# Performance work log

Measured on AMD Instinct MI355X. Metric: run time of the kernel, lower is better.

Reference implementation:

```python
import jax, jax.numpy as jnp
import numpy as np

NEG_SLOPE = 0.2
BN_EPS = 1e-5


def _gatv2(x, src, dst, Wl, Wr, att, b, N, concat):
    # x: [N, Cin]; src/dst: [E] (self-loops already appended)
    H, F = att.shape
    xl = (x @ Wl).reshape(N, H, F)  # source transform
    xr = (x @ Wr).reshape(N, H, F)  # target transform
    s = jax.nn.leaky_relu(xl[src] + xr[dst], NEG_SLOPE)  # [E,H,F]
    e = jnp.einsum('ehf,hf->eh', s, att)                  # [E,H]
    m = jax.ops.segment_max(e, dst, num_segments=N)       # [N,H]
    ex = jnp.exp(e - m[dst])
    den = jax.ops.segment_sum(ex, dst, num_segments=N)
    alpha = ex / den[dst]                                 # [E,H] softmax over in-edges
    out = jax.ops.segment_sum(alpha[:, :, None] * xl[src], dst, num_segments=N)  # [N,H,F]
    out = out.reshape(N, H * F) if concat else out.mean(axis=1)
    return out + b


def _bn_eval(x, g, b, rm, rv):
    return (x - rm) * jax.lax.rsqrt(rv + BN_EPS) * g + b


def setup_inputs() -> dict:
    key = jax.random.key(0)
    ks = jax.random.split(key, 16)
    N, E, Cin, Fh, H, Cout = 50000, 800000, 128, 64, 4, 128
    Hm = H * Fh  # 256
    d = {
        'x': jax.random.normal(ks[0], (N, Cin), jnp.float32),
        'edge_index': jax.random.randint(ks[1], (2, E), 0, N, jnp.int64),
        'Wl1': jax.random.normal(ks[2], (Cin, Hm), jnp.float32) / np.sqrt(Cin),
        'Wr1': jax.random.normal(ks[3], (Cin, Hm), jnp.float32) / np.sqrt(Cin),
        'att1': jax.random.normal(ks[4], (H, Fh), jnp.float32) / np.sqrt(Fh),
        'b1': jnp.zeros((Hm,), jnp.float32),
        'bn1_g': jax.random.uniform(ks[5], (Hm,), jnp.float32, 0.5, 1.5),
        'bn1_b': 0.1 * jax.random.normal(ks[6], (Hm,), jnp.float32),
        'bn1_m': jnp.zeros((Hm,), jnp.float32),
        'bn1_v': jnp.ones((Hm,), jnp.float32),
        'Wl2': jax.random.normal(ks[7], (Hm, Hm), jnp.float32) / np.sqrt(Hm),
        'Wr2': jax.random.normal(ks[8], (Hm, Hm), jnp.float32) / np.sqrt(Hm),
        'att2': jax.random.normal(ks[9], (H, Fh), jnp.float32) / np.sqrt(Fh),
        'b2': jnp.zeros((Hm,), jnp.float32),
        'bn2_g': jax.random.uniform(ks[10], (Hm,), jnp.float32, 0.5, 1.5),
        'bn2_b': 0.1 * jax.random.normal(ks[11], (Hm,), jnp.float32),
        'bn2_m': jnp.zeros((Hm,), jnp.float32),
        'bn2_v': jnp.ones((Hm,), jnp.float32),
        'Wl3': jax.random.normal(ks[12], (Hm, Cout), jnp.float32) / np.sqrt(Hm),
        'Wr3': jax.random.normal(ks[13], (Hm, Cout), jnp.float32) / np.sqrt(Hm),
        'att3': jax.random.normal(ks[14], (1, Cout), jnp.float32) / np.sqrt(Cout),
        'b3': jnp.zeros((Cout,), jnp.float32),
    }
    return d


def reference(x, edge_index, Wl1, Wr1, att1, b1, bn1_g, bn1_b, bn1_m, bn1_v,
              Wl2, Wr2, att2, b2, bn2_g, bn2_b, bn2_m, bn2_v,
              Wl3, Wr3, att3, b3):
    N = x.shape[0]
    loop = jnp.arange(N, dtype=edge_index.dtype)
    src = jnp.concatenate([edge_index[0], loop])  # add self-loops (PyG default)
    dst = jnp.concatenate([edge_index[1], loop])
    h = _gatv2(x, src, dst, Wl1, Wr1, att1, b1, N, True)
    h = jax.nn.elu(_bn_eval(h, bn1_g, bn1_b, bn1_m, bn1_v))  # dropout=identity (eval)
    h = _gatv2(h, src, dst, Wl2, Wr2, att2, b2, N, True)
    h = jax.nn.elu(_bn_eval(h, bn2_g, bn2_b, bn2_m, bn2_v))
    return _gatv2(h, src, dst, Wl3, Wr3, att3, b3, N, False)
```

## Files before the change

### kernel.cpp

```cpp
#include <hip/hip_runtime.h>
#include <math.h>

#define NEG_SLOPE 0.2f
#define BN_EPS 1e-5f
#define LOG2E 1.44269504f

typedef _Float16 f16x8 __attribute__((ext_vector_type(8)));
typedef float f32x4 __attribute__((ext_vector_type(4)));
typedef _Float16 h2 __attribute__((ext_vector_type(2)));

union F8 { f16x8 v; h2 h[4]; _Float16 s[8]; uint4 u; };

__device__ __forceinline__ void async_copy16(const void* g, void* l) {
  __builtin_amdgcn_global_load_lds(
      (const __attribute__((address_space(1))) void*)g,
      (__attribute__((address_space(3))) void*)l, 16, 0, 0);
}

__device__ __forceinline__ unsigned int pack2f(float a, float b) {
  union { unsigned int u; _Float16 h[2]; } c;
  c.h[0] = (_Float16)a; c.h[1] = (_Float16)b; return c.u;
}

__device__ __forceinline__ float fdot2f(h2 a, h2 b, float c) {
#if __has_builtin(__builtin_amdgcn_fdot2)
  return __builtin_amdgcn_fdot2(a, b, c, false);
#else
  return fmaf((float)a[0], (float)b[0], fmaf((float)a[1], (float)b[1], c));
#endif
}

template <int CTRL>
__device__ __forceinline__ float dpp_xadd(float x) {
  int yi = __builtin_amdgcn_mov_dpp(__builtin_bit_cast(int, x), CTRL, 0xF, 0xF, true);
  return x + __builtin_bit_cast(float, yi);
}

__global__ void k_zero_i32(int* __restrict__ p, int n) {
  int i = blockIdx.x * blockDim.x + threadIdx.x;
  if (i < n) p[i] = 0;
}

__global__ void k_f2h(const float* __restrict__ in, unsigned int* __restrict__ out, int n2) {
  int i = blockIdx.x * blockDim.x + threadIdx.x;
  if (i < n2) {
    float2 v = reinterpret_cast<const float2*>(in)[i];
    out[i] = pack2f(v.x, v.y);
  }
}

__global__ __launch_bounds__(256) void k_prep_w3(
    const float* __restrict__ Wl1, const float* __restrict__ Wr1,
    const float* __restrict__ Wl2, const float* __restrict__ Wr2,
    const float* __restrict__ Wl3, const float* __restrict__ Wr3,
    int Cin, int Hm, int Cout,
    _Float16* __restrict__ WT1, _Float16* __restrict__ WT2, _Float16* __restrict__ WT3) {
  int i = blockIdx.x * 256 + threadIdx.x;
  int n1 = 2 * Hm * Cin, n2 = 2 * Hm * Hm, n3 = 2 * Cout * Hm;
  if (i < n1) {
    int c = i / Cin, k = i % Cin;
    float v = (c < Hm) ? Wl1[(size_t)k * Hm + c] : Wr1[(size_t)k * Hm + (c - Hm)];
    WT1[i] = (_Float16)v;
    return;
  }
  i -= n1;
  if (i < n2) {
    int c = i / Hm, k = i % Hm;
    float v = (c < Hm) ? Wl2[(size_t)k * Hm + c] : Wr2[(size_t)k * Hm + (c - Hm)];
    WT2[i] = (_Float16)v;
    return;
  }
  i -= n2;
  if (i < n3) {
    int c = i / Hm, k = i % Hm;
    float v = (c < Cout) ? Wl3[(size_t)k * Cout + c] : Wr3[(size_t)k * Cout + (c - Cout)];
    WT3[i] = (_Float16)v;
  }
}

__global__ __launch_bounds__(256) void k_prep_misc(
    const float* __restrict__ att1, const float* __restrict__ att2, const float* __restrict__ att3,
    const float* __restrict__ b1, const float* __restrict__ g1, const float* __restrict__ bb1,
    const float* __restrict__ m1, const float* __restrict__ v1,
    const float* __restrict__ b2, const float* __restrict__ g2, const float* __restrict__ bb2,
    const float* __restrict__ m2, const float* __restrict__ v2,
    _Float16* __restrict__ a16_1, _Float16* __restrict__ a16_2, _Float16* __restrict__ a16_3,
    float* __restrict__ sc1, float* __restrict__ sh1,
    float* __restrict__ sc2, float* __restrict__ sh2) {
  int c = threadIdx.x;
  a16_1[c] = (_Float16)(att1[c] * LOG2E);
  a16_2[c] = (_Float16)(att2[c] * LOG2E);
  if (c < 128) a16_3[c] = (_Float16)(att3[c] * LOG2E);
  float s = g1[c] * rsqrtf(v1[c] + BN_EPS);
  sc1[c] = s; sh1[c] = (b1[c] - m1[c]) * s + bb1[c];
  s = g2[c] * rsqrtf(v2[c] + BN_EPS);
  sc2[c] = s; sh2[c] = (b2[c] - m2[c]) * s + bb2[c];
}

__global__ void k_count(const int* __restrict__ ei, int E, int N, int* __restrict__ deg) {
  int e = blockIdx.x * blockDim.x + threadIdx.x;
  int T = E + N;
  if (e >= T) return;
  int d = (e < E) ? ei[E + e] : (e - E);
  atomicAdd(&deg[d], 1);
}

__global__ __launch_bounds__(256) void k_bsum(const int* __restrict__ deg, int N,
                                              int* __restrict__ bsum) {
  int t = threadIdx.x;
  int i = blockIdx.x * 256 + t;
  int v = (i < N) ? deg[i] : 0;
  #pragma unroll
  for (int off = 32; off > 0; off >>= 1) v += __shfl_xor(v, off, 64);
  __shared__ int ws[4];
  if ((t & 63) == 0) ws[t >> 6] = v;
  __syncthreads();
  if (t == 0) bsum[blockIdx.x] = ws[0] + ws[1] + ws[2] + ws[3];
}

__global__ __launch_bounds__(1024) void k_bscan(int* __restrict__ bsum, int nb, int N,
                                                int* __restrict__ offs) {
  int t = threadIdx.x;
  int lane = t & 63, w = t >> 6;
  int v = (t < nb) ? bsum[t] : 0;
  int val = v;
  #pragma unroll
  for (int off = 1; off < 64; off <<= 1) {
    int x = __shfl_up(val, off, 64);
    if (lane >= off) val += x;
  }
  __shared__ int ws[16];
  if (lane == 63) ws[w] = val;
  __syncthreads();
  if (w == 0) {
    int s = (lane < 16) ? ws[lane] : 0;
    #pragma unroll
    for (int off = 1; off < 16; off <<= 1) {
      int x = __shfl_up(s, off, 64);
      if (lane >= off) s += x;
    }
    if (lane < 16) ws[lane] = s;
  }
  __syncthreads();
  int excl = (w > 0 ? ws[w - 1] : 0) + val - v;
  if (t < nb) bsum[t] = excl;
  if (t == nb - 1) offs[N] = excl + v;
}

__global__ __launch_bounds__(256) void k_boffs(const int* __restrict__ deg, int N,
                                               const int* __restrict__ bpre,
                                               int* __restrict__ offs, int* __restrict__ cursor) {
  int t = threadIdx.x;
  int i = blockIdx.x * 256 + t;
  int lane = t & 63, w = t >> 6;
  int v = (i < N) ? deg[i] : 0;
  int val = v;
  #pragma unroll
  for (int off = 1; off < 64; off <<= 1) {
    int x = __shfl_up(val, off, 64);
    if (lane >= off) val += x;
  }
  __shared__ int ws[4];
  if (lane == 63) ws[w] = val;
  __syncthreads();
  int wo = 0;
  #pragma unroll
  for (int k = 0; k < 4; ++k) if (k < w) wo += ws[k];
  int excl = bpre[blockIdx.x] + wo + val - v;
  if (i < N) { offs[i] = excl; cursor[i] = excl; }
}

__global__ void k_scatter(const int* __restrict__ ei, int E, int N,
                          int* __restrict__ cursor, int* __restrict__ csr_src) {
  int e = blockIdx.x * blockDim.x + threadIdx.x;
  int T = E + N;
  if (e < 32) csr_src[T + e] = 0;
  if (e >= T) return;
  int s, d;
  if (e < E) { s = ei[e]; d = ei[E + e]; } else { s = d = e - E; }
  int pos = atomicAdd(&cursor[d], 1);
  csr_src[pos] = s;
}

__global__ __launch_bounds__(512) void k_hgemm(const _Float16* __restrict__ A,
                                               const _Float16* __restrict__ BT,
                                               _Float16* __restrict__ C,
                                               int M, int Ntot, int K) {
  __shared__ _Float16 As[2][128 * 64];
  __shared__ _Float16 Bs[2][256 * 64];
  const int t = threadIdx.x;
  const int lane = t & 63, w = t >> 6;
  const int wr = w >> 2, wc = w & 3;
  const int bm0 = blockIdx.x * 128, bn0 = blockIdx.y * 256;
  f32x4 acc[4][4] = {};
  const int nkt = K >> 6;

  auto stage = [&](int b, int kt) {
    #pragma unroll
    for (int i = 0; i < 2; ++i) {
      int q = i * 512 + t;
      int row = q >> 3, sl = q & 7;
      int ssrc = sl ^ (row & 7);
      int ga = bm0 + row; if (ga >= M) ga = M - 1;
      async_copy16(&A[(size_t)ga * K + kt * 64 + ssrc * 8], &As[b][q * 8]);
    }
    #pragma unroll
    for (int i = 0; i < 4; ++i) {
      int q = i * 512 + t;
      int row = q >> 3, sl = q & 7;
      int ssrc = sl ^ (row & 7);
      async_copy16(&BT[(size_t)(bn0 + row) * K + kt * 64 + ssrc * 8], &Bs[b][q * 8]);
    }
  };

  stage(0, 0);
  for (int kt = 0; kt < nkt; ++kt) {
    int cur = kt & 1;
    if (kt + 1 < nkt) {
      stage(cur ^ 1, kt + 1);
      asm volatile("s_waitcnt vmcnt(6)" ::: "memory");
    } else {
      asm volatile("s_waitcnt vmcnt(0)" ::: "memory");
    }
    __builtin_amdgcn_s_barrier();
    #pragma unroll
    for (int ks = 0; ks < 2; ++ks) {
      f16x8 a[4], b[4];
      const int sl = ks * 4 + (lane >> 4);
      #pragma unroll
      for (int mi = 0; mi < 4; ++mi) {
        int row = wr * 64 + mi * 16 + (lane & 15);
        a[mi] = *(const f16x8*)&As[cur][(row * 8 + (sl ^ (row & 7))) * 8];
      }
      #pragma unroll
      for (int ni = 0; ni < 4; ++ni) {
        int row = wc * 64 + ni * 16 + (lane & 15);
        b[ni] = *(const f16x8*)&Bs[cur][(row * 8 + (sl ^ (row & 7))) * 8];
      }
      #pragma unroll
      for (int mi = 0; mi < 4; ++mi)
        #pragma unroll
        for (int ni = 0; ni < 4; ++ni)
          acc[mi][ni] = __builtin_amdgcn_mfma_f32_16x16x32_f16(a[mi], b[ni], acc[mi][ni], 0, 0, 0);
    }
    __builtin_amdgcn_s_barrier();
  }
  const int r0 = (lane >> 4) * 4;
  const int cc = lane & 15;
  #pragma unroll
  for (int mi = 0; mi < 4; ++mi) {
    #pragma unroll
    for (int r = 0; r < 4; ++r) {
      int row = bm0 + wr * 64 + mi * 16 + r0 + r;
      if (row >= M) continue;
      #pragma unroll
      for (int ni = 0; ni < 4; ++ni) {
        int col = bn0 + wc * 64 + ni * 16 + cc;
        C[(size_t)row * Ntot + col] = (_Float16)acc[mi][ni][r];
      }
    }
  }
}

__global__ __launch_bounds__(256) void k_gat4(
    const _Float16* __restrict__ xlr,
    const _Float16* __restrict__ att16,
    const float* __restrict__ sc, const float* __restrict__ sh,
    const int* __restrict__ offs, const int* __restrict__ csr,
    int N, _Float16* __restrict__ hout) {
  const int n = blockIdx.x * 4 + (threadIdx.x >> 6);
  if (n >= N) return;
  const int lane = threadIdx.x & 63;
  const int sub = lane & 15;
  const int qi = lane >> 4;
  const unsigned subB = (unsigned)sub << 5;
  const char* __restrict__ xc = (const char*)xlr;

  F8 at0, at1, xr0, xr1;
  at0.u = *(const uint4*)((const char*)att16 + subB);
  at1.u = *(const uint4*)((const char*)att16 + subB + 16);
  {
    unsigned xro = (unsigned)n * 1024u + 512u + subB;
    xr0.u = *(const uint4*)(xc + xro);
    xr1.u = *(const uint4*)(xc + xro + 16);
  }
  const h2 k02 = {(_Float16)NEG_SLOPE, (_Float16)NEG_SLOPE};
  const int j0 = offs[n], j1 = offs[n + 1];

  float m = -INFINITY, l = 0.f;
  float acc[16];
  #pragma unroll
  for (int i = 0; i < 16; ++i) acc[i] = 0.f;

  unsigned oA = (unsigned)csr[j0 + qi] * 1024u + subB;
  unsigned oB = (unsigned)csr[j0 + 4 + qi] * 1024u + subB;
  F8 v0, v1;
  v0.u = *(const uint4*)(xc + oA);
  v1.u = *(const uint4*)(xc + oA + 16);

  for (int j = j0; j < j1; j += 4) {
    F8 n0, n1;
    n0.u = *(const uint4*)(xc + oB);
    n1.u = *(const uint4*)(xc + oB + 16);
    oB = (unsigned)csr[j + 8 + qi] * 1024u + subB;

    float e = 0.f;
    #pragma unroll
    for (int r = 0; r < 4; ++r) {
      h2 s0 = v0.h[r] + xr0.h[r];
      s0 = __builtin_elementwise_max(s0, s0 * k02);
      e = fdot2f(s0, at0.h[r], e);
      h2 s1 = v1.h[r] + xr1.h[r];
      s1 = __builtin_elementwise_max(s1, s1 * k02);
      e = fdot2f(s1, at1.h[r], e);
    }
    e = dpp_xadd<0xB1>(e);
    e = dpp_xadd<0x4E>(e);
    if (j + qi >= j1) e = -1e30f;

    if (__any(e > m + 11.5f)) {
      float mc = fmaxf(m, e);
      mc = fmaxf(mc, __shfl_xor(mc, 16, 64));
      mc = fmaxf(mc, __shfl_xor(mc, 32, 64));
      float c0 = exp2f(m - mc);
      l *= c0;
      #pragma unroll
      for (int i = 0; i < 16; ++i) acc[i] *= c0;
      m = mc;
    }
    float p = exp2f(e - m);
    l += p;
    #pragma unroll
    for (int i = 0; i < 8; ++i) acc[i] = fmaf(p, (float)v0.s[i], acc[i]);
    #pragma unroll
    for (int i = 0; i < 8; ++i) acc[8 + i] = fmaf(p, (float)v1.s[i], acc[8 + i]);
    v0 = n0; v1 = n1;
  }
  l += __shfl_xor(l, 16, 64);
  l += __shfl_xor(l, 32, 64);
  #pragma unroll
  for (int i = 0; i < 16; ++i) {
    acc[i] += __shfl_xor(acc[i], 16, 64);
    acc[i] += __shfl_xor(acc[i], 32, 64);
  }
  if (qi == 0) {
    float inv = 1.f / l;
    const float4* sc4 = (const float4*)sc;
    const float4* sh4 = (const float4*)sh;
    float ov[16];
    #pragma unroll
    for (int k = 0; k < 4; ++k) {
      float4 s4 = sc4[4 * sub + k], t4 = sh4[4 * sub + k];
      ov[4 * k + 0] = acc[4 * k + 0] * inv * s4.x + t4.x;
      ov[4 * k + 1] = acc[4 * k + 1] * inv * s4.y + t4.y;
      ov[4 * k + 2] = acc[4 * k + 2] * inv * s4.z + t4.z;
      ov[4 * k + 3] = acc[4 * k + 3] * inv * s4.w + t4.w;
    }
    #pragma unroll
    for (int i = 0; i < 16; ++i) ov[i] = ov[i] > 0.f ? ov[i] : (__expf(ov[i]) - 1.f);
    F8 o0, o1;
    #pragma unroll
    for (int i = 0; i < 8; ++i) { o0.s[i] = (_Float16)ov[i]; o1.s[i] = (_Float16)ov[8 + i]; }
    F8* ob = (F8*)hout;
    ob[(size_t)n * 32 + 2 * sub] = o0;
    ob[(size_t)n * 32 + 2 * sub + 1] = o1;
  }
}

__global__ __launch_bounds__(256) void k_gat1(
    const _Float16* __restrict__ xlr,
    const _Float16* __restrict__ att16,
    const float* __restrict__ bias,
    const int* __restrict__ offs, const int* __restrict__ csr,
    int N, float* __restrict__ out) {
  const int n = blockIdx.x * 4 + (threadIdx.x >> 6);
  if (n >= N) return;
  const int lane = threadIdx.x & 63;
  const int sub = lane & 7;
  const int gi = lane >> 3;
  const unsigned subB = (unsigned)sub << 5;
  const char* __restrict__ xc = (const char*)xlr;

  F8 at0, at1, xr0, xr1;
  at0.u = *(const uint4*)((const char*)att16 + subB);
  at1.u = *(const uint4*)((const char*)att16 + subB + 16);
  {
    unsigned xro = (unsigned)n * 512u + 256u + subB;
    xr0.u = *(const uint4*)(xc + xro);
    xr1.u = *(const uint4*)(xc + xro + 16);
  }
  const h2 k02 = {(_Float16)NEG_SLOPE, (_Float16)NEG_SLOPE};
  const int j0 = offs[n], j1 = offs[n + 1];

  float m = -INFINITY, l = 0.f;
  float acc[16];
  #pragma unroll
  for (int i = 0; i < 16; ++i) acc[i] = 0.f;

  unsigned oA = (unsigned)csr[j0 + gi] * 512u + subB;
  unsigned oB = (unsigned)csr[j0 + 8 + gi] * 512u + subB;
  F8 v0, v1;
  v0.u = *(const uint4*)(xc + oA);
  v1.u = *(const uint4*)(xc + oA + 16);

  for (int j = j0; j < j1; j += 8) {
    F8 n0, n1;
    n0.u = *(const uint4*)(xc + oB);
    n1.u = *(const uint4*)(xc + oB + 16);
    oB = (unsigned)csr[j + 16 + gi] * 512u + subB;

    float e = 0.f;
    #pragma unroll
    for (int r = 0; r < 4; ++r) {
      h2 s0 = v0.h[r] + xr0.h[r];
      s0 = __builtin_elementwise_max(s0, s0 * k02);
      e = fdot2f(s0, at0.h[r], e);
      h2 s1 = v1.h[r] + xr1.h[r];
      s1 = __builtin_elementwise_max(s1, s1 * k02);
      e = fdot2f(s1, at1.h[r], e);
    }
    e = dpp_xadd<0xB1>(e);
    e = dpp_xadd<0x4E>(e);
    e += __shfl_xor(e, 4, 64);
    if (j + gi >= j1) e = -1e30f;

    if (__any(e > m + 11.5f)) {
      float mc = fmaxf(m, e);
      mc = fmaxf(mc, __shfl_xor(mc, 8, 64));
      mc = fmaxf(mc, __shfl_xor(mc, 16, 64));
      mc = fmaxf(mc, __shfl_xor(mc, 32, 64));
      float c0 = exp2f(m - mc);
      l *= c0;
      #pragma unroll
      for (int i = 0; i < 16; ++i) acc[i] *= c0;
      m = mc;
    }
    float p = exp2f(e - m);
    l += p;
    #pragma unroll
    for (int i = 0; i < 8; ++i) acc[i] = fmaf(p, (float)v0.s[i], acc[i]);
    #pragma unroll
    for (int i = 0; i < 8; ++i) acc[8 + i] = fmaf(p, (float)v1.s[i], acc[8 + i]);
    v0 = n0; v1 = n1;
  }
  l += __shfl_xor(l, 8, 64);
  l += __shfl_xor(l, 16, 64);
  l += __shfl_xor(l, 32, 64);
  #pragma unroll
  for (int i = 0; i < 16; ++i) {
    acc[i] += __shfl_xor(acc[i], 8, 64);
    acc[i] += __shfl_xor(acc[i], 16, 64);
    acc[i] += __shfl_xor(acc[i], 32, 64);
  }
  if (gi == 0) {
    float inv = 1.f / l;
    const float4* b4 = (const float4*)bias;
    float4* ob = (float4*)out;
    #pragma unroll
    for (int k = 0; k < 4; ++k) {
      float4 bb = b4[4 * sub + k];
      float4 o;
      o.x = acc[4 * k + 0] * inv + bb.x;
      o.y = acc[4 * k + 1] * inv + bb.y;
      o.z = acc[4 * k + 2] * inv + bb.z;
      o.w = acc[4 * k + 3] * inv + bb.w;
      ob[(size_t)n * 32 + 4 * sub + k] = o;
    }
  }
}

extern "C" void kernel_launch(void* const* d_in, const int* in_sizes, int n_in,
                              void* d_out, int out_size, void* d_ws, size_t ws_size,
                              hipStream_t stream) {
  const float* x    = (const float*)d_in[0];
  const int*   ei   = (const int*)d_in[1];
  const float* Wl1  = (const float*)d_in[2];
  const float* Wr1  = (const float*)d_in[3];
  const float* att1 = (const float*)d_in[4];
  const float* b1   = (const float*)d_in[5];
  const float* bn1g = (const float*)d_in[6];
  const float* bn1b = (const float*)d_in[7];
  const float* bn1m = (const float*)d_in[8];
  const float* bn1v = (const float*)d_in[9];
  const float* Wl2  = (const float*)d_in[10];
  const float* Wr2  = (const float*)d_in[11];
  const float* att2 = (const float*)d_in[12];
  const float* b2   = (const float*)d_in[13];
  const float* bn2g = (const float*)d_in[14];
  const float* bn2b = (const float*)d_in[15];
  const float* bn2m = (const float*)d_in[16];
  const float* bn2v = (const float*)d_in[17];
  const float* Wl3  = (const float*)d_in[18];
  const float* Wr3  = (const float*)d_in[19];
  const float* att3 = (const float*)d_in[20];
  const float* b3   = (const float*)d_in[21];

  const int Hm   = in_sizes[5];
  const int Cout = in_sizes[21];
  const int Cin  = in_sizes[2] / Hm;
  const int N    = in_sizes[0] / Cin;
  const int E    = in_sizes[1] / 2;
  const int T    = E + N;

  _Float16* x16 = (_Float16*)d_ws;
  _Float16* h   = x16 + (size_t)N * Cin;
  _Float16* xlr = h + (size_t)N * Hm;
  _Float16* WT1 = xlr + (size_t)N * 2 * Hm;
  _Float16* WT2 = WT1 + (size_t)2 * Hm * Cin;
  _Float16* WT3 = WT2 + (size_t)2 * Hm * Hm;
  _Float16* a16_1 = WT3 + (size_t)2 * Cout * Hm;
  _Float16* a16_2 = a16_1 + 256;
  _Float16* a16_3 = a16_2 + 256;
  float* sc1 = (float*)(a16_3 + 128);
  float* sh1 = sc1 + 256;
  float* sc2 = sh1 + 256;
  float* sh2 = sc2 + 256;
  int* deg    = (int*)(sh2 + 256);
  int* offs   = deg + N;
  int* cursor = offs + N + 1;
  int* csr    = cursor + N;
  int* bsum   = csr + T + 32;

  const int nb = (N + 255) / 256;

  k_zero_i32<<<(N + 255) / 256, 256, 0, stream>>>(deg, N);
  k_count<<<(T + 255) / 256, 256, 0, stream>>>(ei, E, N, deg);
  k_bsum<<<nb, 256, 0, stream>>>(deg, N, bsum);
  k_bscan<<<1, 1024, 0, stream>>>(bsum, nb, N, offs);
  k_boffs<<<nb, 256, 0, stream>>>(deg, N, bsum, offs, cursor);
  k_scatter<<<(T + 255) / 256, 256, 0, stream>>>(ei, E, N, cursor, csr);

  int n2 = N * Cin / 2;
  k_f2h<<<(n2 + 255) / 256, 256, 0, stream>>>(x, (unsigned int*)x16, n2);
  int wtot = 2 * Hm * Cin + 2 * Hm * Hm + 2 * Cout * Hm;
  k_prep_w3<<<(wtot + 255) / 256, 256, 0, stream>>>(Wl1, Wr1, Wl2, Wr2, Wl3, Wr3,
                                                    Cin, Hm, Cout, WT1, WT2, WT3);
  k_prep_misc<<<1, 256, 0, stream>>>(att1, att2, att3,
                                     b1, bn1g, bn1b, bn1m, bn1v,
                                     b2, bn2g, bn2b, bn2m, bn2v,
                                     a16_1, a16_2, a16_3, sc1, sh1, sc2, sh2);

  const int mb = (N + 127) / 128;
  const int gb = (N + 3) / 4;

  k_hgemm<<<dim3(mb, 2 * Hm / 256), 512, 0, stream>>>(x16, WT1, xlr, N, 2 * Hm, Cin);
  k_gat4<<<gb, 256, 0, stream>>>(xlr, a16_1, sc1, sh1, offs, csr, N, h);

  k_hgemm<<<dim3(mb, 2 * Hm / 256), 512, 0, stream>>>(h, WT2, xlr, N, 2 * Hm, Hm);
  k_gat4<<<gb, 256, 0, stream>>>(xlr, a16_2, sc2, sh2, offs, csr, N, h);

  k_hgemm<<<dim3(mb, 2 * Cout / 256), 512, 0, stream>>>(h, WT3, xlr, N, 2 * Cout, Hm);
  k_gat1<<<gb, 256, 0, stream>>>(xlr, a16_3, b3, offs, csr, N, (float*)d_out);
}
```

Measured before the change: 377.8 us.

## Schedule GAT nodes by descending degree and fuse prep kernels

Result: slower. 699.8 us (+85.2%).

```diff
diff --git a/kernel.cpp b/kernel.cpp
--- a/kernel.cpp
+++ b/kernel.cpp
@@ -36,49 +36,13 @@
   return x + __builtin_bit_cast(float, yi);
 }
 
-__global__ void k_zero_i32(int* __restrict__ p, int n) {
-  int i = blockIdx.x * blockDim.x + threadIdx.x;
-  if (i < n) p[i] = 0;
-}
-
-__global__ void k_f2h(const float* __restrict__ in, unsigned int* __restrict__ out, int n2) {
-  int i = blockIdx.x * blockDim.x + threadIdx.x;
-  if (i < n2) {
-    float2 v = reinterpret_cast<const float2*>(in)[i];
-    out[i] = pack2f(v.x, v.y);
-  }
-}
-
-__global__ __launch_bounds__(256) void k_prep_w3(
+__global__ __launch_bounds__(256) void k_prep_all(
+    const float* __restrict__ x, unsigned int* __restrict__ x16u, int n2,
     const float* __restrict__ Wl1, const float* __restrict__ Wr1,
     const float* __restrict__ Wl2, const float* __restrict__ Wr2,
     const float* __restrict__ Wl3, const float* __restrict__ Wr3,
     int Cin, int Hm, int Cout,
-    _Float16* __restrict__ WT1, _Float16* __restrict__ WT2, _Float16* __restrict__ WT3) {
-  int i = blockIdx.x * 256 + threadIdx.x;
-  int n1 = 2 * Hm * Cin, n2 = 2 * Hm * Hm, n3 = 2 * Cout * Hm;
-  if (i < n1) {
-    int c = i / Cin, k = i % Cin;
-    float v = (c < Hm) ? Wl1[(size_t)k * Hm + c] : Wr1[(size_t)k * Hm + (c - Hm)];
-    WT1[i] = (_Float16)v;
-    return;
-  }
-  i -= n1;
-  if (i < n2) {
-    int c = i / Hm, k = i % Hm;
-    float v = (c < Hm) ? Wl2[(size_t)k * Hm + c] : Wr2[(size_t)k * Hm + (c - Hm)];
-    WT2[i] = (_Float16)v;
-    return;
-  }
-  i -= n2;
-  if (i < n3) {
-    int c = i / Hm, k = i % Hm;
-    float v = (c < Cout) ? Wl3[(size_t)k * Cout + c] : Wr3[(size_t)k * Cout + (c - Cout)];
-    WT3[i] = (_Float16)v;
-  }
-}
-
-__global__ __launch_bounds__(256) void k_prep_misc(
+    _Float16* __restrict__ WT1, _Float16* __restrict__ WT2, _Float16* __restrict__ WT3,
     const float* __restrict__ att1, const float* __restrict__ att2, const float* __restrict__ att3,
     const float* __restrict__ b1, const float* __restrict__ g1, const float* __restrict__ bb1,
     const float* __restrict__ m1, const float* __restrict__ v1,
@@ -87,14 +51,45 @@
     _Float16* __restrict__ a16_1, _Float16* __restrict__ a16_2, _Float16* __restrict__ a16_3,
     float* __restrict__ sc1, float* __restrict__ sh1,
     float* __restrict__ sc2, float* __restrict__ sh2) {
-  int c = threadIdx.x;
-  a16_1[c] = (_Float16)(att1[c] * LOG2E);
-  a16_2[c] = (_Float16)(att2[c] * LOG2E);
-  if (c < 128) a16_3[c] = (_Float16)(att3[c] * LOG2E);
-  float s = g1[c] * rsqrtf(v1[c] + BN_EPS);
-  sc1[c] = s; sh1[c] = (b1[c] - m1[c]) * s + bb1[c];
-  s = g2[c] * rsqrtf(v2[c] + BN_EPS);
-  sc2[c] = s; sh2[c] = (b2[c] - m2[c]) * s + bb2[c];
+  int i = blockIdx.x * 256 + threadIdx.x;
+  if (i < n2) {
+    float2 v = reinterpret_cast<const float2*>(x)[i];
+    x16u[i] = pack2f(v.x, v.y);
+    return;
+  }
+  i -= n2;
+  int w1 = 2 * Hm * Cin, w2 = 2 * Hm * Hm, w3 = 2 * Cout * Hm;
+  if (i < w1) {
+    int c = i / Cin, k = i % Cin;
+    float v = (c < Hm) ? Wl1[(size_t)k * Hm + c] : Wr1[(size_t)k * Hm + (c - Hm)];
+    WT1[i] = (_Float16)v;
+    return;
+  }
+  i -= w1;
+  if (i < w2) {
+    int c = i / Hm, k = i % Hm;
+    float v = (c < Hm) ? Wl2[(size_t)k * Hm + c] : Wr2[(size_t)k * Hm + (c - Hm)];
+    WT2[i] = (_Float16)v;
+    return;
+  }
+  i -= w2;
+  if (i < w3) {
+    int c = i / Hm, k = i % Hm;
+    float v = (c < Cout) ? Wl3[(size_t)k * Cout + c] : Wr3[(size_t)k * Cout + (c - Cout)];
+    WT3[i] = (_Float16)v;
+    return;
+  }
+  i -= w3;
+  if (i < 256) {
+    int c = i;
+    a16_1[c] = (_Float16)(att1[c] * LOG2E);
+    a16_2[c] = (_Float16)(att2[c] * LOG2E);
+    if (c < 128) a16_3[c] = (_Float16)(att3[c] * LOG2E);
+    float s = g1[c] * rsqrtf(v1[c] + BN_EPS);
+    sc1[c] = s; sh1[c] = (b1[c] - m1[c]) * s + bb1[c];
+    s = g2[c] * rsqrtf(v2[c] + BN_EPS);
+    sc2[c] = s; sh2[c] = (b2[c] - m2[c]) * s + bb2[c];
+  }
 }
 
 __global__ void k_count(const int* __restrict__ ei, int E, int N, int* __restrict__ deg) {
@@ -144,7 +139,7 @@
   __syncthreads();
   int excl = (w > 0 ? ws[w - 1] : 0) + val - v;
   if (t < nb) bsum[t] = excl;
-  if (t == nb - 1) offs[N] = excl + v;
+  if (t == nb - 1 && offs) offs[N] = excl + v;
 }
 
 __global__ __launch_bounds__(256) void k_boffs(const int* __restrict__ deg, int N,
@@ -180,6 +175,22 @@
   if (e < E) { s = ei[e]; d = ei[E + e]; } else { s = d = e - E; }
   int pos = atomicAdd(&cursor[d], 1);
   csr_src[pos] = s;
+}
+
+__global__ void k_hist(const int* __restrict__ deg, int N, int* __restrict__ hist) {
+  int i = blockIdx.x * blockDim.x + threadIdx.x;
+  if (i >= N) return;
+  int b = 1023 - min(deg[i], 1023);
+  atomicAdd(&hist[b], 1);
+}
+
+__global__ void k_horder(const int* __restrict__ deg, int N,
+                         int* __restrict__ hcur, int* __restrict__ order) {
+  int i = blockIdx.x * blockDim.x + threadIdx.x;
+  if (i >= N) return;
+  int b = 1023 - min(deg[i], 1023);
+  int pos = atomicAdd(&hcur[b], 1);
+  order[pos] = i;
 }
 
 __global__ __launch_bounds__(512) void k_hgemm(const _Float16* __restrict__ A,
@@ -267,9 +278,11 @@
     const _Float16* __restrict__ att16,
     const float* __restrict__ sc, const float* __restrict__ sh,
     const int* __restrict__ offs, const int* __restrict__ csr,
+    const int* __restrict__ order,
     int N, _Float16* __restrict__ hout) {
-  const int n = blockIdx.x * 4 + (threadIdx.x >> 6);
-  if (n >= N) return;
+  const int idx = blockIdx.x * 4 + (threadIdx.x >> 6);
+  if (idx >= N) return;
+  const int n = order[idx];
   const int lane = threadIdx.x & 63;
   const int sub = lane & 15;
   const int qi = lane >> 4;
@@ -358,12 +371,12 @@
     }
     #pragma unroll
     for (int i = 0; i < 16; ++i) ov[i] = ov[i] > 0.f ? ov[i] : (__expf(ov[i]) - 1.f);
-    F8 o0, o1;
-    #pragma unroll
-    for (int i = 0; i < 8; ++i) { o0.s[i] = (_Float16)ov[i]; o1.s[i] = (_Float16)ov[8 + i]; }
+    F8 o0h, o1h;
+    #pragma unroll
+    for (int i = 0; i < 8; ++i) { o0h.s[i] = (_Float16)ov[i]; o1h.s[i] = (_Float16)ov[8 + i]; }
     F8* ob = (F8*)hout;
-    ob[(size_t)n * 32 + 2 * sub] = o0;
-    ob[(size_t)n * 32 + 2 * sub + 1] = o1;
+    ob[(size_t)n * 32 + 2 * sub] = o0h;
+    ob[(size_t)n * 32 + 2 * sub + 1] = o1h;
   }
 }
 
@@ -372,9 +385,11 @@
     const _Float16* __restrict__ att16,
     const float* __restrict__ bias,
     const int* __restrict__ offs, const int* __restrict__ csr,
+    const int* __restrict__ order,
     int N, float* __restrict__ out) {
-  const int n = blockIdx.x * 4 + (threadIdx.x >> 6);
-  if (n >= N) return;
+  const int idx = blockIdx.x * 4 + (threadIdx.x >> 6);
+  if (idx >= N) return;
+  const int n = order[idx];
   const int lane = threadIdx.x & 63;
   const int sub = lane & 7;
   const int gi = lane >> 3;
@@ -520,35 +535,42 @@
   int* cursor = offs + N + 1;
   int* csr    = cursor + N;
   int* bsum   = csr + T + 32;
+  int* hist   = bsum + (N + 255) / 256;
+  int* order  = hist + 1024;
 
   const int nb = (N + 255) / 256;
 
-  k_zero_i32<<<(N + 255) / 256, 256, 0, stream>>>(deg, N);
+  hipMemsetAsync(deg, 0, (size_t)N * sizeof(int), stream);
+  hipMemsetAsync(hist, 0, 1024 * sizeof(int), stream);
   k_count<<<(T + 255) / 256, 256, 0, stream>>>(ei, E, N, deg);
   k_bsum<<<nb, 256, 0, stream>>>(deg, N, bsum);
   k_bscan<<<1, 1024, 0, stream>>>(bsum, nb, N, offs);
   k_boffs<<<nb, 256, 0, stream>>>(deg, N, bsum, offs, cursor);
   k_scatter<<<(T + 255) / 256, 256, 0, stream>>>(ei, E, N, cursor, csr);
+  k_hist<<<(N + 255) / 256, 256, 0, stream>>>(deg, N, hist);
+  k_bscan<<<1, 1024, 0, stream>>>(hist, 1024, 0, (int*)nullptr);
+  k_horder<<<(N + 255) / 256, 256, 0, stream>>>(deg, N, hist, order);
 
   int n2 = N * Cin / 2;
-  k_f2h<<<(n2 + 255) / 256, 256, 0, stream>>>(x, (unsigned int*)x16, n2);
   int wtot = 2 * Hm * Cin + 2 * Hm * Hm + 2 * Cout * Hm;
-  k_prep_w3<<<(wtot + 255) / 256, 256, 0, stream>>>(Wl1, Wr1, Wl2, Wr2, Wl3, Wr3,
-                                                    Cin, Hm, Cout, WT1, WT2, WT3);
-  k_prep_misc<<<1, 256, 0, stream>>>(att1, att2, att3,
-                                     b1, bn1g, bn1b, bn1m, bn1v,
-                                     b2, bn2g, bn2b, bn2m, bn2v,
-                                     a16_1, a16_2, a16_3, sc1, sh1, sc2, sh2);
+  int ptot = n2 + wtot + 256;
+  k_prep_all<<<(ptot + 255) / 256, 256, 0, stream>>>(
+      x, (unsigned int*)x16, n2,
+      Wl1, Wr1, Wl2, Wr2, Wl3, Wr3, Cin, Hm, Cout, WT1, WT2, WT3,
+      att1, att2, att3,
+      b1, bn1g, bn1b, bn1m, bn1v,
+      b2, bn2g, bn2b, bn2m, bn2v,
+      a16_1, a16_2, a16_3, sc1, sh1, sc2, sh2);
 
   const int mb = (N + 127) / 128;
   const int gb = (N + 3) / 4;
 
   k_hgemm<<<dim3(mb, 2 * Hm / 256), 512, 0, stream>>>(x16, WT1, xlr, N, 2 * Hm, Cin);
-  k_gat4<<<gb, 256, 0, stream>>>(xlr, a16_1, sc1, sh1, offs, csr, N, h);
+  k_gat4<<<gb, 256, 0, stream>>>(xlr, a16_1, sc1, sh1, offs, csr, order, N, h);
 
   k_hgemm<<<dim3(mb, 2 * Hm / 256), 512, 0, stream>>>(h, WT2, xlr, N, 2 * Hm, Hm);
-  k_gat4<<<gb, 256, 0, stream>>>(xlr, a16_2, sc2, sh2, offs, csr, N, h);
+  k_gat4<<<gb, 256, 0, stream>>>(xlr, a16_2, sc2, sh2, offs, csr, order, N, h);
 
   k_hgemm<<<dim3(mb, 2 * Cout / 256), 512, 0, stream>>>(h, WT3, xlr, N, 2 * Cout, Hm);
-  k_gat1<<<gb, 256, 0, stream>>>(xlr, a16_3, b3, offs, csr, N, (float*)d_out);
-}
+  k_gat1<<<gb, 256, 0, stream>>>(xlr, a16_3, b3, offs, csr, order, N, (float*)d_out);
+}
```
